# Kernel tuning notes

Measured on AMD Instinct MI355X. Metric: run time of the kernel, lower is better.

Reference implementation:

```python
import jax, jax.numpy as jnp
import numpy as np

EPSILON = 0.01            # params.epsilon (cluster precision regularizer)
GAMMA = 0.005             # params.gamma (outlier/uniform component weight)
FIX_CLUSTER_POS_ITER = 1  # params.fix_cluster_pos_iter


def _sqdist(TVs, X):
    # TVs: (M, 3, N) transformed points, X: (K, 3) cluster means -> (M, N, K)
    return ((TVs ** 2).sum(1)[:, :, None]
            + (X ** 2).sum(1)[None, None, :]
            - 2.0 * jnp.einsum('mdn,kd->mnk', TVs, X))


def setup_inputs() -> dict:
    key = jax.random.key(0)
    kV, kX, kQ = jax.random.split(key, 3)
    M, N, K = 8, 8192, 256
    Vs = jax.random.normal(kV, (M, 3, N), dtype=jnp.float32)      # 3D point clouds
    X0 = jax.random.normal(kX, (K, 3), dtype=jnp.float32)         # init cluster means (sphere init)
    Q0 = 0.1 + 0.2 * jax.random.uniform(kQ, (K,), dtype=jnp.float32)  # init cluster precisions
    return {"Vs": Vs, "X0": X0, "Q0": Q0, "num_iters": 6}


def reference(Vs, X0, Q0, num_iters):
    M, _, N = Vs.shape
    K = X0.shape[0]
    dtype = Vs.dtype

    # mean_init: init_R = I, init_t = -mean(V) per view
    t0 = -Vs.mean(axis=2, keepdims=True)          # (M, 3, 1)
    TVs = Vs + t0
    beta = GAMMA * jnp.mean(Q0) ** 1.5            # get_default_beta(Q, gamma)

    X, Q = X0, Q0
    ds = _sqdist(TVs, X)                          # (M, N, K)
    R = jnp.broadcast_to(jnp.eye(3, dtype=dtype), (M, 3, 3))
    t = t0[:, :, 0]

    for i in range(num_iters):
        if i != num_iters - 1:  # detach everything except backprop_iter = [last]
            X = jax.lax.stop_gradient(X)
            Q = jax.lax.stop_gradient(Q)
            ds = jax.lax.stop_gradient(ds)

        # E-step: soft posteriors with uniform outlier component beta
        ap = jnp.exp(-0.5 * ds * Q) * Q ** 1.5    # (M, N, K); priors = 1, pyz_feature = 1
        a = ap / (ap.sum(axis=-1, keepdims=True) + beta)

        # M-step: weighted sufficient statistics
        L = a.sum(axis=1)                                   # (M, K)
        W = jnp.einsum('mdn,mnk->mdk', Vs, a) * Q           # (M, 3, K)
        mW = W.sum(axis=-1)                                 # (M, 3)
        b = L * Q                                           # (M, K)
        mX = jnp.einsum('mk,kd->md', b, X)                  # (M, 3)
        z = b.sum(axis=-1)                                  # (M,)

        # P = (W @ X)^T - mX mW^T / z  : 3x3 weighted cross-covariance per view
        P = (jnp.einsum('mdk,ke->med', W, X)
             - mX[:, :, None] * mW[:, None, :] / z[:, None, None])

        # batched Procrustes: R = U diag(1,1,det(U V^T)) V^T
        U, _, Vt = jnp.linalg.svd(P)
        det = jnp.linalg.det(jnp.einsum('mij,mjk->mik', U, Vt))
        sgn = jnp.concatenate([jnp.ones((M, 2), dtype), det[:, None]], axis=1)
        R = jnp.einsum('mij,mjk->mik', U * sgn[:, None, :], Vt)   # (M, 3, 3)
        t = (mX - jnp.einsum('mij,mj->mi', R, mW)) / z[:, None]   # (M, 3)
        TVs = jnp.einsum('mij,mjn->min', R, Vs) + t[:, :, None]   # (M, 3, N)

        # shared cluster updates (sum over views)
        den = L.sum(axis=0)                                 # (K,)
        if i > FIX_CLUSTER_POS_ITER:
            X = jnp.einsum('mdn,mnk->kd', TVs, a) / den[:, None]
        ds = _sqdist(TVs, X)
        wn = (a * ds).sum(axis=(0, 1))                      # (K,)
        Q = 3.0 * den / (wn + 3.0 * den * EPSILON)

    return TVs, R, t, X
```

## Files before the change

kernel.cpp:

```cpp
#include <hip/hip_runtime.h>
#include <math.h>

#define Mv 8
#define Nv 8192
#define Kv 256
#define BPM 64
#define NBLK (Mv*BPM)
#define NPB (Nv/BPM)
#define NITER 6
#define EPSILON_C 0.01f
#define GAMMA_C 0.005f

#define SWZK(k) ((((k)&63)<<2)|((k)>>6))
#define SWZP(p) ((((p)&31)<<2)|((p)>>5))

#define AC_STATS 0
#define AC_L     128
#define AC_W     2176
#define AC_H     8320
#define ACCSZ    10368

__device__ __forceinline__ float wave_red_sum(float x) {
  int v;
  float t;
  v = __builtin_bit_cast(int, x);
  t = __builtin_bit_cast(float, __builtin_amdgcn_update_dpp(0, v, 0x111, 0xf, 0xf, true));
  x += t; v = __builtin_bit_cast(int, x);
  t = __builtin_bit_cast(float, __builtin_amdgcn_update_dpp(0, v, 0x112, 0xf, 0xf, true));
  x += t; v = __builtin_bit_cast(int, x);
  t = __builtin_bit_cast(float, __builtin_amdgcn_update_dpp(0, v, 0x114, 0xf, 0xf, true));
  x += t; v = __builtin_bit_cast(int, x);
  t = __builtin_bit_cast(float, __builtin_amdgcn_update_dpp(0, v, 0x118, 0xf, 0xf, true));
  x += t; v = __builtin_bit_cast(int, x);
  t = __builtin_bit_cast(float, __builtin_amdgcn_update_dpp(0, v, 0x142, 0xa, 0xf, false));
  x += t; v = __builtin_bit_cast(int, x);
  t = __builtin_bit_cast(float, __builtin_amdgcn_update_dpp(0, v, 0x143, 0xc, 0xf, false));
  x += t;
  return __builtin_bit_cast(float, __builtin_amdgcn_readlane(__builtin_bit_cast(int, x), 63));
}

__device__ __forceinline__ float quad_red_sum(float x) {
  int v = __builtin_bit_cast(int, x);
  float t = __builtin_bit_cast(float, __builtin_amdgcn_update_dpp(0, v, 0xB1, 0xf, 0xf, true));
  x += t; v = __builtin_bit_cast(int, x);
  t = __builtin_bit_cast(float, __builtin_amdgcn_update_dpp(0, v, 0x4E, 0xf, 0xf, true));
  x += t;
  return x;
}

__device__ __forceinline__ float sel4(int c, float a0, float a1, float a2, float a3) {
  float r = a0;
  r = (c==1) ? a1 : r;
  r = (c==2) ? a2 : r;
  r = (c==3) ? a3 : r;
  return r;
}

#define JROTF(app,aqq,apq,apr,aqr, vp0,vp1,vp2, vq0,vq1,vq2) do {           \
    float tau_ = (aqq - app) * __builtin_amdgcn_rcpf(2.0f*apq);             \
    float tt_ = __builtin_amdgcn_rcpf(fabsf(tau_) +                         \
                   __builtin_amdgcn_sqrtf(fmaf(tau_,tau_,1.0f)));           \
    tt_ = (tau_ < 0.0f) ? -tt_ : tt_;                                       \
    tt_ = (apq == 0.0f) ? 0.0f : tt_;                                       \
    float c_ = __builtin_amdgcn_rsqf(fmaf(tt_,tt_,1.0f)), s_ = tt_*c_;      \
    float papq_ = apq;                                                      \
    app = fmaf(-tt_,papq_,app); aqq = fmaf(tt_,papq_,aqq); apq = 0.0f;      \
    float tp_ = apr, tq_ = aqr;                                             \
    apr = c_*tp_ - s_*tq_; aqr = s_*tp_ + c_*tq_;                           \
    tp_=vp0; tq_=vq0; vp0=c_*tp_-s_*tq_; vq0=s_*tp_+c_*tq_;                 \
    tp_=vp1; tq_=vq1; vp1=c_*tp_-s_*tq_; vq1=s_*tp_+c_*tq_;                 \
    tp_=vp2; tq_=vq2; vp2=c_*tp_-s_*tq_; vq2=s_*tp_+c_*tq_;                 \
  } while(0)

#define CSWAP3F(la,lb, a0,a1,a2, b0,b1,b2) do {                             \
    if (la < lb) { float t_;                                                \
      t_=la; la=lb; lb=t_; t_=a0; a0=b0; b0=t_;                             \
      t_=a1; a1=b1; b1=t_; t_=a2; a2=b2; b2=t_; }                           \
  } while(0)

template<int ITPREV>
__device__ __forceinline__ void small_update(const float* __restrict__ acc,
                                             const float* __restrict__ X0,
                                             int tid,
                                             float (*sX)[3], float* sQ,
                                             float (*sR)[9], float (*sT)[3],
                                             float* sTn) {
  const int k = tid;
  float lk[Mv], w0v[Mv], w1v[Mv], w2v[Mv], hk[Mv];
  #pragma unroll
  for (int mm=0;mm<Mv;mm++) {
    lk[mm]  = acc[AC_L + mm*Kv + k];
    w0v[mm] = acc[AC_W + (mm*3+0)*Kv + k];
    w1v[mm] = acc[AC_W + (mm*3+1)*Kv + k];
    w2v[mm] = acc[AC_W + (mm*3+2)*Kv + k];
    hk[mm]  = acc[AC_H + mm*Kv + k];
  }
  float xp0 = 0.f, xp1 = 0.f, xp2 = 0.f;
  if (ITPREV <= 1) {
    xp0 = X0[k*3+0]; xp1 = X0[k*3+1]; xp2 = X0[k*3+2];
  }

  if (tid < Mv) {
    int mm = tid;
    const float* st = acc + AC_STATS + mm*16;
    float s0=st[0], s1=st[1], s2v=st[2], s3=st[3], s4=st[4], s5=st[5],
          s6=st[6], s7=st[7], s8=st[8], s9=st[9], s10=st[10], s11=st[11],
          s12=st[12], s13=st[13], s14=st[14], s15=st[15];
    float z = s0;
    float mX0 = s1, mX1 = s2v, mX2 = s3;
    float mW0 = s4, mW1 = s5, mW2 = s6;
    float iz = __builtin_amdgcn_rcpf(z);
    float P00 = s7  - mX0*mW0*iz;
    float P01 = s8  - mX0*mW1*iz;
    float P02 = s9  - mX0*mW2*iz;
    float P10 = s10 - mX1*mW0*iz;
    float P11 = s11 - mX1*mW1*iz;
    float P12 = s12 - mX1*mW2*iz;
    float P20 = s13 - mX2*mW0*iz;
    float P21 = s14 - mX2*mW1*iz;
    float P22 = s15 - mX2*mW2*iz;
    float a00 = P00*P00 + P10*P10 + P20*P20;
    float a01 = P00*P01 + P10*P11 + P20*P21;
    float a02 = P00*P02 + P10*P12 + P20*P22;
    float a11 = P01*P01 + P11*P11 + P21*P21;
    float a12 = P01*P02 + P11*P12 + P21*P22;
    float a22 = P02*P02 + P12*P12 + P22*P22;
    float v00=1, v01=0, v02=0, v10=0, v11=1, v12=0, v20=0, v21=0, v22=1;
    #pragma unroll 1
    for (int sweep = 0; sweep < 5; sweep++) {
      JROTF(a00,a11,a01, a02,a12, v00,v10,v20, v01,v11,v21);
      JROTF(a00,a22,a02, a01,a12, v00,v10,v20, v02,v12,v22);
      JROTF(a11,a22,a12, a01,a02, v01,v11,v21, v02,v12,v22);
    }
    float l0 = a00, l1 = a11, l2 = a22;
    CSWAP3F(l0,l1, v00,v10,v20, v01,v11,v21);
    CSWAP3F(l1,l2, v01,v11,v21, v02,v12,v22);
    CSWAP3F(l0,l1, v00,v10,v20, v01,v11,v21);
    float detP = P00*(P11*P22-P12*P21) - P01*(P10*P22-P12*P20)
               + P02*(P10*P21-P11*P20);
    float s2d = (detP < 0.0f) ? -1.0f : 1.0f;
    float tiny = 1e-18f*l0 + 1e-30f;
    float w0i = __builtin_amdgcn_rsqf(fmaxf(l0,tiny));
    float w1i = __builtin_amdgcn_rsqf(fmaxf(l1,tiny));
    float w2i = s2d*__builtin_amdgcn_rsqf(fmaxf(l2,tiny));
    float M00 = w0i*v00*v00 + w1i*v01*v01 + w2i*v02*v02;
    float M01 = w0i*v00*v10 + w1i*v01*v11 + w2i*v02*v12;
    float M02 = w0i*v00*v20 + w1i*v01*v21 + w2i*v02*v22;
    float M11 = w0i*v10*v10 + w1i*v11*v11 + w2i*v12*v12;
    float M12 = w0i*v10*v20 + w1i*v11*v21 + w2i*v12*v22;
    float M22 = w0i*v20*v20 + w1i*v21*v21 + w2i*v22*v22;
    float R00n = P00*M00 + P01*M01 + P02*M02;
    float R01n = P00*M01 + P01*M11 + P02*M12;
    float R02n = P00*M02 + P01*M12 + P02*M22;
    float R10n = P10*M00 + P11*M01 + P12*M02;
    float R11n = P10*M01 + P11*M11 + P12*M12;
    float R12n = P10*M02 + P11*M12 + P12*M22;
    float R20n = P20*M00 + P21*M01 + P22*M02;
    float R21n = P20*M01 + P21*M11 + P22*M12;
    float R22n = P20*M02 + P21*M12 + P22*M22;
    float tm0 = (mX0 - (R00n*mW0 + R01n*mW1 + R02n*mW2))*iz;
    float tm1 = (mX1 - (R10n*mW0 + R11n*mW1 + R12n*mW2))*iz;
    float tm2 = (mX2 - (R20n*mW0 + R21n*mW1 + R22n*mW2))*iz;
    sR[mm][0]=R00n; sR[mm][1]=R01n; sR[mm][2]=R02n;
    sR[mm][3]=R10n; sR[mm][4]=R11n; sR[mm][5]=R12n;
    sR[mm][6]=R20n; sR[mm][7]=R21n; sR[mm][8]=R22n;
    sT[mm][0]=tm0; sT[mm][1]=tm1; sT[mm][2]=tm2;
    sTn[mm] = tm0*tm0 + tm1*tm1 + tm2*tm2;
  }
  __syncthreads();
  {
    float den = 0.f, Xn0=0.f, Xn1=0.f, Xn2=0.f, S2=0.f;
    #pragma unroll
    for (int mm=0;mm<Mv;mm++) {
      float r0 = sR[mm][0]*w0v[mm] + sR[mm][1]*w1v[mm] + sR[mm][2]*w2v[mm];
      float r1 = sR[mm][3]*w0v[mm] + sR[mm][4]*w1v[mm] + sR[mm][5]*w2v[mm];
      float r2 = sR[mm][6]*w0v[mm] + sR[mm][7]*w1v[mm] + sR[mm][8]*w2v[mm];
      float tt0 = sT[mm][0], tt1 = sT[mm][1], tt2 = sT[mm][2];
      den += lk[mm];
      Xn0 += r0 + tt0*lk[mm]; Xn1 += r1 + tt1*lk[mm]; Xn2 += r2 + tt2*lk[mm];
      S2  += hk[mm] + 2.f*(tt0*r0+tt1*r1+tt2*r2) + sTn[mm]*lk[mm];
    }
    float x0, x1, x2;
    if (ITPREV > 1) { float inv = __builtin_amdgcn_rcpf(den);
                      x0=Xn0*inv; x1=Xn1*inv; x2=Xn2*inv; }
    else            { x0=xp0; x1=xp1; x2=xp2; }
    float wn = S2 + (x0*x0+x1*x1+x2*x2)*den - 2.f*(x0*Xn0+x1*Xn1+x2*Xn2);
    float qn = 3.f*den / (wn + 3.f*den*EPSILON_C);
    sX[k][0]=x0; sX[k][1]=x1; sX[k][2]=x2;
    sQ[k] = qn;
  }
}

template<int IT>
__global__ __launch_bounds__(256) void p_iter(const float* __restrict__ Vs,
                                              const float* __restrict__ X0,
                                              const float* __restrict__ Q0,
                                              float* __restrict__ ws) {
  __shared__ __align__(16) float sC4[Kv][4];
  __shared__ float sKC[Kv];
  __shared__ __align__(16) float sP4[NPB][4];
  __shared__ __align__(16) float sV4[NPB][4];
  __shared__ float sLi[NPB];
  __shared__ float st4[4][16];
  __shared__ float sX[Kv][3];
  __shared__ float sQ[Kv];
  __shared__ float sR[Mv][9];
  __shared__ float sT[Mv][3];
  __shared__ float sTn[Mv];
  __shared__ float sredq[4];
  __shared__ float sredt[12];

  int tid  = threadIdx.x;
  int wave = tid >> 6, lane = tid & 63;
  int bid  = blockIdx.x;
  int m    = bid / BPM;
  int blk  = bid % BPM;
  int n0   = blk * NPB;

  float* acc  = ws + (IT % 3)*ACCSZ;
  float* accz = ws + ((IT+1) % 3)*ACCSZ;

  const float* V0 = Vs + (size_t)(m*3+0)*Nv;
  const float* V1 = Vs + (size_t)(m*3+1)*Nv;
  const float* V2 = Vs + (size_t)(m*3+2)*Nv;
  float vx=0.f, vy=0.f, vz=0.f;
  if (tid < NPB) {
    int n = n0 + tid;
    vx = V0[n]; vy = V1[n]; vz = V2[n];
  }
  float q_own = Q0[tid];
  { float s = wave_red_sum(q_own);
    if (lane == 0) sredq[wave] = s; }

  float t00=0.f, t01=0.f, t02=0.f;
  if (IT == 0) {
    float sx=0.f, sy=0.f, sz=0.f;
    for (int n = tid; n < Nv; n += 256) { sx += V0[n]; sy += V1[n]; sz += V2[n]; }
    sx = wave_red_sum(sx); sy = wave_red_sum(sy); sz = wave_red_sum(sz);
    if (lane == 0) { sredt[wave] = sx; sredt[4+wave] = sy; sredt[8+wave] = sz; }
    sX[tid][0] = X0[3*tid+0];
    sX[tid][1] = X0[3*tid+1];
    sX[tid][2] = X0[3*tid+2];
    sQ[tid]    = q_own;
    __syncthreads();
    t00 = -(sredt[0]+sredt[1]+sredt[2]+sredt[3]) * (1.f/(float)Nv);
    t01 = -(sredt[4]+sredt[5]+sredt[6]+sredt[7]) * (1.f/(float)Nv);
    t02 = -(sredt[8]+sredt[9]+sredt[10]+sredt[11]) * (1.f/(float)Nv);
  } else {
    const float* accp = ws + ((IT+2) % 3)*ACCSZ;
    small_update<(IT > 0) ? (IT-1) : 0>(accp, X0, tid, sX, sQ, sR, sT, sTn);
    __syncthreads();
  }
  float beta;
  { float mq = (sredq[0]+sredq[1]+sredq[2]+sredq[3]) * (1.f/(float)Kv);
    beta = GAMMA_C * mq * sqrtf(mq); }

  if (IT < NITER-1) {
    int base = bid*21;
    if (tid < 21 && base + tid < ACCSZ) accz[base + tid] = 0.f;
  }

  float R00,R01,R02,R10,R11,R12,R20,R21,R22, t0,t1,t2;
  if (IT == 0) {
    R00=1;R01=0;R02=0; R10=0;R11=1;R12=0; R20=0;R21=0;R22=1;
    t0=t00; t1=t01; t2=t02;
  } else {
    R00=sR[m][0];R01=sR[m][1];R02=sR[m][2];
    R10=sR[m][3];R11=sR[m][4];R12=sR[m][5];
    R20=sR[m][6];R21=sR[m][7];R22=sR[m][8];
    t0=sT[m][0]; t1=sT[m][1]; t2=sT[m][2];
  }

  const float L2E = 1.4426950408889634f;
  {
    float xx = sX[tid][0], xy = sX[tid][1], xz = sX[tid][2];
    float q  = sQ[tid];
    float qL = q * L2E;
    float kA = -0.5f*qL;
    float kB = kA*(xx*xx+xy*xy+xz*xz);
    float kQ32 = q*sqrtf(q);
    int rr = SWZK(tid);
    *reinterpret_cast<float4*>(&sC4[rr][0]) = make_float4(qL*xx, qL*xy, qL*xz, kA);
    sKC[rr] = kQ32 * __builtin_amdgcn_exp2f(kB);
  }
  if (tid < NPB) {
    float px = fmaf(R00,vx, fmaf(R01,vy, fmaf(R02,vz, t0)));
    float py = fmaf(R10,vx, fmaf(R11,vy, fmaf(R12,vz, t1)));
    float pz = fmaf(R20,vx, fmaf(R21,vy, fmaf(R22,vz, t2)));
    float tvn = fmaf(px,px, fmaf(py,py, pz*pz));
    float vn  = fmaf(vx,vx, fmaf(vy,vy, vz*vz));
    int pr = SWZP(tid);
    *reinterpret_cast<float4*>(&sP4[pr][0]) = make_float4(px,py,pz,tvn);
    *reinterpret_cast<float4*>(&sV4[pr][0]) = make_float4(vx,vy,vz,vn);
  }
  __syncthreads();

  {
    int ks = tid & 3, pg = tid >> 2;
    float4 P0 = *reinterpret_cast<const float4*>(&sP4[SWZP(2*pg+0)][0]);
    float4 P1 = *reinterpret_cast<const float4*>(&sP4[SWZP(2*pg+1)][0]);
    float s0 = 0.f, s1 = 0.f;
    #pragma unroll 4
    for (int j = 0; j < Kv/4; j++) {
      int row = (j<<2) | ks;
      float4 c4 = *reinterpret_cast<const float4*>(&sC4[row][0]);
      float kc = sKC[row];
      float a0 = fmaf(P0.x,c4.x, fmaf(P0.y,c4.y, fmaf(P0.z,c4.z, P0.w*c4.w)));
      float a1 = fmaf(P1.x,c4.x, fmaf(P1.y,c4.y, fmaf(P1.z,c4.z, P1.w*c4.w)));
      s0 = fmaf(__builtin_amdgcn_exp2f(a0), kc, s0);
      s1 = fmaf(__builtin_amdgcn_exp2f(a1), kc, s1);
    }
    float S0 = quad_red_sum(s0);
    float S1 = quad_red_sum(s1);
    if (ks < 2) {
      float Ssel = (ks == 1) ? S1 : S0;
      sLi[SWZP(2*pg + ks)] = -__log2f(Ssel + beta);
    }
  }
  __syncthreads();

  float cXx0,cXy0,cXz0,cA0,cC0, cXx1,cXy1,cXz1,cA1,cC1,
        cXx2,cXy2,cXz2,cA2,cC2, cXx3,cXy3,cXz3,cA3,cC3;
  {
    int kg = tid >> 2;
    #define LDC(c) { int rr = SWZK(4*kg + c); \
      float4 t4 = *reinterpret_cast<const float4*>(&sC4[rr][0]); \
      cXx##c=t4.x; cXy##c=t4.y; cXz##c=t4.z; cA##c=t4.w; cC##c=sKC[rr]; }
    LDC(0) LDC(1) LDC(2) LDC(3)
    #undef LDC
  }
  float L0=0,L1=0,L2=0,L3=0, Wx0=0,Wx1=0,Wx2=0,Wx3=0,
        Wy0=0,Wy1=0,Wy2=0,Wy3=0, Wz0=0,Wz1=0,Wz2=0,Wz3=0,
        H0=0,H1=0,H2=0,H3=0;
  {
    int ns = tid & 3;
    #pragma unroll 4
    for (int j = 0; j < NPB/4; j++) {
      int prow = (j<<2) | ns;
      float4 p4 = *reinterpret_cast<const float4*>(&sP4[prow][0]);
      float4 v4 = *reinterpret_cast<const float4*>(&sV4[prow][0]);
      float li = sLi[prow];
      #define P2K(c) { \
        float arg = fmaf(p4.w, cA##c, li); \
        arg = fmaf(p4.x, cXx##c, fmaf(p4.y, cXy##c, fmaf(p4.z, cXz##c, arg))); \
        float e = __builtin_amdgcn_exp2f(arg) * cC##c; \
        L##c += e; \
        Wx##c = fmaf(e, v4.x, Wx##c); Wy##c = fmaf(e, v4.y, Wy##c); \
        Wz##c = fmaf(e, v4.z, Wz##c); H##c  = fmaf(e, v4.w, H##c); }
      P2K(0) P2K(1) P2K(2) P2K(3)
      #undef P2K
    }
  }
  L0=quad_red_sum(L0); L1=quad_red_sum(L1); L2=quad_red_sum(L2); L3=quad_red_sum(L3);
  Wx0=quad_red_sum(Wx0); Wx1=quad_red_sum(Wx1); Wx2=quad_red_sum(Wx2); Wx3=quad_red_sum(Wx3);
  Wy0=quad_red_sum(Wy0); Wy1=quad_red_sum(Wy1); Wy2=quad_red_sum(Wy2); Wy3=quad_red_sum(Wy3);
  Wz0=quad_red_sum(Wz0); Wz1=quad_red_sum(Wz1); Wz2=quad_red_sum(Wz2); Wz3=quad_red_sum(Wz3);
  H0=quad_red_sum(H0); H1=quad_red_sum(H1); H2=quad_red_sum(H2); H3=quad_red_sum(H3);
  int c = tid & 3;
  float vL  = sel4(c, L0,L1,L2,L3);
  float vWx = sel4(c, Wx0,Wx1,Wx2,Wx3);
  float vWy = sel4(c, Wy0,Wy1,Wy2,Wy3);
  float vWz = sel4(c, Wz0,Wz1,Wz2,Wz3);
  float vH  = sel4(c, H0,H1,H2,H3);
  atomicAdd(&acc[AC_L + m*Kv + tid], vL);
  atomicAdd(&acc[AC_W + (m*3+0)*Kv + tid], vWx);
  atomicAdd(&acc[AC_W + (m*3+1)*Kv + tid], vWy);
  atomicAdd(&acc[AC_W + (m*3+2)*Kv + tid], vWz);
  atomicAdd(&acc[AC_H + m*Kv + tid], vH);

  {
    float q  = sQ[tid];
    float x0 = sX[tid][0], x1 = sX[tid][1], x2 = sX[tid][2];
    float bk = vL*q;
    float sw0 = vWx*q, sw1 = vWy*q, sw2 = vWz*q;
    float pr[16];
    pr[0]=bk;  pr[1]=bk*x0; pr[2]=bk*x1; pr[3]=bk*x2;
    pr[4]=sw0; pr[5]=sw1;   pr[6]=sw2;
    pr[7]=sw0*x0;  pr[8]=sw1*x0;  pr[9]=sw2*x0;
    pr[10]=sw0*x1; pr[11]=sw1*x1; pr[12]=sw2*x1;
    pr[13]=sw0*x2; pr[14]=sw1*x2; pr[15]=sw2*x2;
    float red[16];
    #pragma unroll
    for (int v2=0; v2<16; v2++) red[v2] = wave_red_sum(pr[v2]);
    if (lane == 0) {
      #pragma unroll
      for (int v2=0; v2<16; v2++) st4[wave][v2] = red[v2];
    }
    __syncthreads();
    if (tid < 16)
      atomicAdd(&acc[AC_STATS + m*16 + ((tid + blk) & 15)],
                st4[0][(tid+blk)&15]+st4[1][(tid+blk)&15]+
                st4[2][(tid+blk)&15]+st4[3][(tid+blk)&15]);
  }
}

#define OUT_TOTAL (Mv*3*Nv + 72 + 24 + Kv*3)
__global__ __launch_bounds__(256) void p3_final(const float* __restrict__ Vs,
                                                const float* __restrict__ X0,
                                                const float* __restrict__ ws,
                                                float* __restrict__ out) {
  __shared__ float sX[Kv][3];
  __shared__ float sQ[Kv];
  __shared__ float sR[Mv][9];
  __shared__ float sT[Mv][3];
  __shared__ float sTn[Mv];
  int tid = threadIdx.x;
  const float* acc = ws + ((NITER-1) % 3)*ACCSZ;
  small_update<NITER-1>(acc, X0, tid, sX, sQ, sR, sT, sTn);
  __syncthreads();

  for (int idx = blockIdx.x*256 + tid; idx < OUT_TOTAL; idx += 256*256) {
    if (idx < Mv*3*Nv) {
      int m = idx / (3*Nv);
      int r = idx % (3*Nv);
      int d = r / Nv;
      int n = r % Nv;
      float vx = Vs[(size_t)(m*3+0)*Nv + n];
      float vy = Vs[(size_t)(m*3+1)*Nv + n];
      float vz = Vs[(size_t)(m*3+2)*Nv + n];
      out[idx] = fmaf(sR[m][d*3+0],vx,
                 fmaf(sR[m][d*3+1],vy,
                 fmaf(sR[m][d*3+2],vz, sT[m][d])));
    } else {
      int j = idx - Mv*3*Nv;
      float v;
      if (j < 72)      v = ((float*)sR)[j];
      else if (j < 96) v = ((float*)sT)[j-72];
      else             v = ((float*)sX)[j-96];
      out[idx] = v;
    }
  }
}

extern "C" void kernel_launch(void* const* d_in, const int* in_sizes, int n_in,
                              void* d_out, int out_size, void* d_ws, size_t ws_size,
                              hipStream_t stream) {
  const float* Vs = (const float*)d_in[0];
  const float* X0 = (const float*)d_in[1];
  const float* Q0 = (const float*)d_in[2];
  float* out = (float*)d_out;
  float* ws  = (float*)d_ws;

  hipMemsetAsync(ws, 0, ACCSZ * sizeof(float), stream);
  p_iter<0><<<NBLK, 256, 0, stream>>>(Vs, X0, Q0, ws);
  p_iter<1><<<NBLK, 256, 0, stream>>>(Vs, X0, Q0, ws);
  p_iter<2><<<NBLK, 256, 0, stream>>>(Vs, X0, Q0, ws);
  p_iter<3><<<NBLK, 256, 0, stream>>>(Vs, X0, Q0, ws);
  p_iter<4><<<NBLK, 256, 0, stream>>>(Vs, X0, Q0, ws);
  p_iter<5><<<NBLK, 256, 0, stream>>>(Vs, X0, Q0, ws);
  p3_final<<<256, 256, 0, stream>>>(Vs, X0, ws, out);
}
```

Measured before the change: 175.3 us.

## Double blocks per view and split atomic accumulators into two buffers

Doubles the blocks per view so each block handles half as many points, and rewrites the log-sum-exp stage to give one point per quad. Each iteration's accumulator buffer is split into two halves chosen by block parity, which halves atomic contention; readers now sum both halves. A launch-bounds occupancy hint is also added. In exchange, every block does more redundant global reads in the per-block small update, and the per-block fixed setup cost is paid twice as often.

```diff
diff --git a/kernel.cpp b/kernel.cpp
--- a/kernel.cpp
+++ b/kernel.cpp
@@ -4,7 +4,7 @@
 #define Mv 8
 #define Nv 8192
 #define Kv 256
-#define BPM 64
+#define BPM 128
 #define NBLK (Mv*BPM)
 #define NPB (Nv/BPM)
 #define NITER 6
@@ -12,13 +12,16 @@
 #define GAMMA_C 0.005f
 
 #define SWZK(k) ((((k)&63)<<2)|((k)>>6))
-#define SWZP(p) ((((p)&31)<<2)|((p)>>5))
+#define SWZP(p) ((((p)&15)<<2)|((p)>>4))
 
 #define AC_STATS 0
 #define AC_L     128
 #define AC_W     2176
 #define AC_H     8320
 #define ACCSZ    10368
+#define BUFSZ    (2*ACCSZ)
+
+#define ALD2(accp, off) ((accp)[off] + (accp)[(off)+ACCSZ])
 
 __device__ __forceinline__ float wave_red_sum(float x) {
   int v;
@@ -89,11 +92,11 @@
   float lk[Mv], w0v[Mv], w1v[Mv], w2v[Mv], hk[Mv];
   #pragma unroll
   for (int mm=0;mm<Mv;mm++) {
-    lk[mm]  = acc[AC_L + mm*Kv + k];
-    w0v[mm] = acc[AC_W + (mm*3+0)*Kv + k];
-    w1v[mm] = acc[AC_W + (mm*3+1)*Kv + k];
-    w2v[mm] = acc[AC_W + (mm*3+2)*Kv + k];
-    hk[mm]  = acc[AC_H + mm*Kv + k];
+    lk[mm]  = ALD2(acc, AC_L + mm*Kv + k);
+    w0v[mm] = ALD2(acc, AC_W + (mm*3+0)*Kv + k);
+    w1v[mm] = ALD2(acc, AC_W + (mm*3+1)*Kv + k);
+    w2v[mm] = ALD2(acc, AC_W + (mm*3+2)*Kv + k);
+    hk[mm]  = ALD2(acc, AC_H + mm*Kv + k);
   }
   float xp0 = 0.f, xp1 = 0.f, xp2 = 0.f;
   if (ITPREV <= 1) {
@@ -102,10 +105,13 @@
 
   if (tid < Mv) {
     int mm = tid;
-    const float* st = acc + AC_STATS + mm*16;
-    float s0=st[0], s1=st[1], s2v=st[2], s3=st[3], s4=st[4], s5=st[5],
-          s6=st[6], s7=st[7], s8=st[8], s9=st[9], s10=st[10], s11=st[11],
-          s12=st[12], s13=st[13], s14=st[14], s15=st[15];
+    const int sb = AC_STATS + mm*16;
+    float s0=ALD2(acc,sb+0), s1=ALD2(acc,sb+1), s2v=ALD2(acc,sb+2),
+          s3=ALD2(acc,sb+3), s4=ALD2(acc,sb+4), s5=ALD2(acc,sb+5),
+          s6=ALD2(acc,sb+6), s7=ALD2(acc,sb+7), s8=ALD2(acc,sb+8),
+          s9=ALD2(acc,sb+9), s10=ALD2(acc,sb+10), s11=ALD2(acc,sb+11),
+          s12=ALD2(acc,sb+12), s13=ALD2(acc,sb+13), s14=ALD2(acc,sb+14),
+          s15=ALD2(acc,sb+15);
     float z = s0;
     float mX0 = s1, mX1 = s2v, mX2 = s3;
     float mW0 = s4, mW1 = s5, mW2 = s6;
@@ -192,10 +198,10 @@
 }
 
 template<int IT>
-__global__ __launch_bounds__(256) void p_iter(const float* __restrict__ Vs,
-                                              const float* __restrict__ X0,
-                                              const float* __restrict__ Q0,
-                                              float* __restrict__ ws) {
+__global__ __launch_bounds__(256, 4) void p_iter(const float* __restrict__ Vs,
+                                                 const float* __restrict__ X0,
+                                                 const float* __restrict__ Q0,
+                                                 float* __restrict__ ws) {
   __shared__ __align__(16) float sC4[Kv][4];
   __shared__ float sKC[Kv];
   __shared__ __align__(16) float sP4[NPB][4];
@@ -217,8 +223,8 @@
   int blk  = bid % BPM;
   int n0   = blk * NPB;
 
-  float* acc  = ws + (IT % 3)*ACCSZ;
-  float* accz = ws + ((IT+1) % 3)*ACCSZ;
+  float* acc  = ws + (IT % 3)*BUFSZ + (blk & 1)*ACCSZ;
+  float* accz = ws + ((IT+1) % 3)*BUFSZ;
 
   const float* V0 = Vs + (size_t)(m*3+0)*Nv;
   const float* V1 = Vs + (size_t)(m*3+1)*Nv;
@@ -247,7 +253,7 @@
     t01 = -(sredt[4]+sredt[5]+sredt[6]+sredt[7]) * (1.f/(float)Nv);
     t02 = -(sredt[8]+sredt[9]+sredt[10]+sredt[11]) * (1.f/(float)Nv);
   } else {
-    const float* accp = ws + ((IT+2) % 3)*ACCSZ;
+    const float* accp = ws + ((IT+2) % 3)*BUFSZ;
     small_update<(IT > 0) ? (IT-1) : 0>(accp, X0, tid, sX, sQ, sR, sT, sTn);
     __syncthreads();
   }
@@ -257,7 +263,7 @@
 
   if (IT < NITER-1) {
     int base = bid*21;
-    if (tid < 21 && base + tid < ACCSZ) accz[base + tid] = 0.f;
+    if (tid < 21 && base + tid < BUFSZ) accz[base + tid] = 0.f;
   }
 
   float R00,R01,R02,R10,R11,R12,R20,R21,R22, t0,t1,t2;
@@ -297,25 +303,18 @@
 
   {
     int ks = tid & 3, pg = tid >> 2;
-    float4 P0 = *reinterpret_cast<const float4*>(&sP4[SWZP(2*pg+0)][0]);
-    float4 P1 = *reinterpret_cast<const float4*>(&sP4[SWZP(2*pg+1)][0]);
-    float s0 = 0.f, s1 = 0.f;
+    float4 P0 = *reinterpret_cast<const float4*>(&sP4[SWZP(pg)][0]);
+    float s0 = 0.f;
     #pragma unroll 4
     for (int j = 0; j < Kv/4; j++) {
       int row = (j<<2) | ks;
       float4 c4 = *reinterpret_cast<const float4*>(&sC4[row][0]);
       float kc = sKC[row];
       float a0 = fmaf(P0.x,c4.x, fmaf(P0.y,c4.y, fmaf(P0.z,c4.z, P0.w*c4.w)));
-      float a1 = fmaf(P1.x,c4.x, fmaf(P1.y,c4.y, fmaf(P1.z,c4.z, P1.w*c4.w)));
       s0 = fmaf(__builtin_amdgcn_exp2f(a0), kc, s0);
-      s1 = fmaf(__builtin_amdgcn_exp2f(a1), kc, s1);
     }
     float S0 = quad_red_sum(s0);
-    float S1 = quad_red_sum(s1);
-    if (ks < 2) {
-      float Ssel = (ks == 1) ? S1 : S0;
-      sLi[SWZP(2*pg + ks)] = -__log2f(Ssel + beta);
-    }
+    if (ks == 0) sLi[SWZP(pg)] = -__log2f(S0 + beta);
   }
   __syncthreads();
 
@@ -405,7 +404,7 @@
   __shared__ float sT[Mv][3];
   __shared__ float sTn[Mv];
   int tid = threadIdx.x;
-  const float* acc = ws + ((NITER-1) % 3)*ACCSZ;
+  const float* acc = ws + ((NITER-1) % 3)*BUFSZ;
   small_update<NITER-1>(acc, X0, tid, sX, sQ, sR, sT, sTn);
   __syncthreads();
 
@@ -441,7 +440,7 @@
   float* out = (float*)d_out;
   float* ws  = (float*)d_ws;
 
-  hipMemsetAsync(ws, 0, ACCSZ * sizeof(float), stream);
+  hipMemsetAsync(ws, 0, BUFSZ * sizeof(float), stream);
   p_iter<0><<<NBLK, 256, 0, stream>>>(Vs, X0, Q0, ws);
   p_iter<1><<<NBLK, 256, 0, stream>>>(Vs, X0, Q0, ws);
   p_iter<2><<<NBLK, 256, 0, stream>>>(Vs, X0, Q0, ws);
```

Result: slower. 220.4 us (+25.7%).
